# Optimization experiments

Hardware: AMD Instinct MI355X
Metric: run time of the kernel (lower is better)

The kernel has to match this reference:

```python
import jax, jax.numpy as jnp
import numpy as np

HEADS = 8


def setup_inputs() -> dict:
    key = jax.random.key(0)
    k1, k2, k3, k4, k5 = jax.random.split(key, 5)
    bt, b_sz, n, dim = 2, 4, 1024, 512
    inner6 = 3072  # inner_dim * 6 where inner_dim = heads * dim_head = 512
    return {
        "x": jax.random.normal(k1, (bt, b_sz, n, dim), dtype=jnp.float32),
        "W_qkv": jax.random.normal(k2, (dim, inner6), dtype=jnp.float32) * 0.02,
        "b_qkv": jax.random.normal(k3, (inner6,), dtype=jnp.float32) * 0.02,
        "W_out": jax.random.normal(k4, (1024, dim), dtype=jnp.float32) * 0.02,
        "b_out": jax.random.normal(k5, (dim,), dtype=jnp.float32) * 0.02,
    }


def reference(x, W_qkv, b_qkv, W_out, b_out):
    bt, b_sz, n, dim = x.shape
    # to_qkv: Linear(dim, 3072) -> reshape (bt,b,n,3,H,hd) -> transpose(2,4)
    qkv = (x @ W_qkv + b_qkv).reshape(bt, b_sz, n, 3, HEADS, -1)
    qkv = qkv.transpose(0, 1, 4, 3, 2, 5)  # (bt, b, H, 3, n, hd)
    q, k, v = qkv[:, :, :, 0], qkv[:, :, :, 1], qkv[:, :, :, 2]
    scale = (dim // HEADS) ** -0.5  # faithful: uses dim//heads, not per-head width
    attn = jax.nn.softmax(jnp.einsum("abhnd,abhmd->abhnm", q * scale, k), axis=-1)
    out = jnp.einsum("abhnm,abhmd->abhnd", attn, v)
    out = out.transpose(0, 1, 3, 2, 4).reshape(bt, b_sz, n, -1)  # (bt,b,n,H*hd)
    return out @ W_out + b_out
```

## Files before the change

kernel.cpp:

```cpp
#include <hip/hip_runtime.h>

typedef __attribute__((ext_vector_type(4))) float f32x4;
typedef __attribute__((ext_vector_type(16))) float f32x16;
typedef __attribute__((ext_vector_type(8))) __bf16 bf16x8;
typedef __attribute__((ext_vector_type(8))) unsigned short ushortx8;
typedef unsigned short u16;
typedef unsigned int u32;

#define AS1 __attribute__((address_space(1)))
#define AS3 __attribute__((address_space(3)))

__device__ __forceinline__ void gld_lds16(const void* g, void* s) {
  __builtin_amdgcn_global_load_lds((AS1 void*)g, (AS3 void*)s, 16, 0, 0);
}

__device__ __forceinline__ u16 f2bf(float f) {
  unsigned int u = __float_as_uint(f);
  unsigned int r = (u + 0x7FFFu + ((u >> 16) & 1u)) >> 16;
  return (u16)r;
}

#define QSCALE 0.1803368801111244f

__global__ void cvt_f32_bf16(const float* __restrict__ src, u16* __restrict__ dst, int n) {
  int i = (blockIdx.x * blockDim.x + threadIdx.x) * 8;
  if (i >= n) return;
  const float4 a = *(const float4*)&src[i];
  const float4 b = *(const float4*)&src[i + 4];
  ushortx8 o;
  o[0] = f2bf(a.x); o[1] = f2bf(a.y); o[2] = f2bf(a.z); o[3] = f2bf(a.w);
  o[4] = f2bf(b.x); o[5] = f2bf(b.y); o[6] = f2bf(b.z); o[7] = f2bf(b.w);
  *(ushortx8*)&dst[i] = o;
}

__global__ void scale_bias(const float* __restrict__ src, float* __restrict__ dst, int n,
                           int boundary, float s) {
  int i = blockIdx.x * blockDim.x + threadIdx.x;
  if (i < n) dst[i] = src[i] * (i < boundary ? s : 1.0f);
}

__global__ void transpose_to_bf16(const float* __restrict__ src, u16* __restrict__ dst,
                                  int R, int C, int boundary, float s) {
  __shared__ float tile[32][33];
  const int c0 = blockIdx.x * 32, r0 = blockIdx.y * 32;
  const int tx = threadIdx.x, ty = threadIdx.y;
  #pragma unroll
  for (int i = ty; i < 32; i += 8)
    tile[i][tx] = src[(size_t)(r0 + i) * C + c0 + tx];
  __syncthreads();
  #pragma unroll
  for (int i = ty; i < 32; i += 8) {
    const float sc = (c0 + i < boundary) ? s : 1.0f;
    dst[(size_t)(c0 + i) * R + r0 + tx] = f2bf(tile[tx][i] * sc);
  }
}

__global__ void transpose_v(const u16* __restrict__ qkv, u16* __restrict__ vt) {
  __shared__ u16 tile[32][34];
  const int bh = blockIdx.z, b = bh >> 3, h = bh & 7;
  const int n0 = blockIdx.y * 32, d0 = blockIdx.x * 32;
  const int tx = threadIdx.x, ty = threadIdx.y;
  const u16* src = qkv + (size_t)(b * 1024) * 3072 + 2048 + h * 128;
  #pragma unroll
  for (int i = ty; i < 32; i += 8)
    tile[i][tx] = src[(size_t)(n0 + i) * 3072 + d0 + tx];
  __syncthreads();
  u16* dst = vt + (size_t)(b * 8 + h) * 128 * 1024;
  #pragma unroll
  for (int i = ty; i < 32; i += 8)
    dst[(size_t)(d0 + i) * 1024 + n0 + tx] = tile[tx][i];
}

template <int BM, int BN, int BK, int OUT_BF16>
__global__ __launch_bounds__(256, 4) void gemm_bt(const u16* __restrict__ A,
                                                  const u16* __restrict__ Bt,
                                                  const float* __restrict__ bias,
                                                  void* __restrict__ Cv,
                                                  int M, int N, int K) {
  constexpr int RPC = 512 / BK;
  constexpr int LPR = BK / 8;
  constexpr int MASK = LPR - 1;
  constexpr int P = 64 / BK > 0 ? 64 / BK : 1;
  constexpr int CA = BM / RPC, CB = BN / RPC;
  constexpr int CAW = CA / 4, CBW = CB / 4;
  constexpr int VM = CAW + CBW;
  constexpr int FM = BM / 32, FN = BN / 32;
  constexpr int KS = BK / 32;

  __shared__ __attribute__((aligned(16))) u16 As[2][BM * BK];
  __shared__ __attribute__((aligned(16))) u16 Bs[2][BN * BK];
  const int nwg = gridDim.x * gridDim.y;
  int bid = blockIdx.y * gridDim.x + blockIdx.x;
  if ((nwg & 7) == 0) bid = (bid & 7) * (nwg >> 3) + (bid >> 3);
  const int n0 = (bid % gridDim.x) * BN, m0 = (bid / gridDim.x) * BM;
  const int tid = threadIdx.x;
  const int w = tid >> 6, l = tid & 63;
  const int wr = w >> 1, wc = w & 1;
  const int lr = l >> 4, lc = l & 15;
  f32x4 acc[FM][FN] = {};

#define GSTAGE(bi, k0)                                                          \
  do {                                                                          \
    _Pragma("unroll") for (int i = 0; i < CAW; ++i) {                           \
      const int c = w * CAW + i;                                                \
      const int row = c * RPC + l / LPR;                                        \
      const int col = ((l % LPR) ^ ((row / P) & MASK)) * 8;                     \
      gld_lds16(&A[(size_t)(m0 + row) * K + (k0) + col], &As[bi][c * 512]);     \
    }                                                                           \
    _Pragma("unroll") for (int i = 0; i < CBW; ++i) {                           \
      const int c = w * CBW + i;                                                \
      const int row = c * RPC + l / LPR;                                        \
      const int col = ((l % LPR) ^ ((row / P) & MASK)) * 8;                     \
      gld_lds16(&Bt[(size_t)(n0 + row) * K + (k0) + col], &Bs[bi][c * 512]);    \
    }                                                                           \
  } while (0)

#define GCOMP(bi)                                                                      \
  do {                                                                                 \
    _Pragma("unroll") for (int ks = 0; ks < KS; ++ks) {                                \
      bf16x8 af[FM], bfr[FN];                                                          \
      _Pragma("unroll") for (int m = 0; m < FM; ++m) {                                 \
        const int row = wr * (BM / 2) + m * 16 + lc;                                   \
        af[m] = *(const bf16x8*)&As[bi][row * BK +                                     \
                                        (((ks * 4 + lr) ^ ((row / P) & MASK)) << 3)];  \
      }                                                                                \
      _Pragma("unroll") for (int n = 0; n < FN; ++n) {                                 \
        const int row = wc * (BN / 2) + n * 16 + lc;                                   \
        bfr[n] = *(const bf16x8*)&Bs[bi][row * BK +                                    \
                                         (((ks * 4 + lr) ^ ((row / P) & MASK)) << 3)]; \
      }                                                                                \
      __builtin_amdgcn_s_setprio(1);                                                   \
      _Pragma("unroll") for (int m = 0; m < FM; ++m)                                   \
          _Pragma("unroll") for (int n = 0; n < FN; ++n)                               \
              acc[m][n] =                                                              \
          __builtin_amdgcn_mfma_f32_16x16x32_bf16(af[m], bfr[n], acc[m][n], 0, 0, 0);  \
      __builtin_amdgcn_s_setprio(0);                                                   \
    }                                                                                  \
  } while (0)

  GSTAGE(0, 0);
  int buf = 0;
  for (int k0 = BK; k0 < K; k0 += BK) {
    GSTAGE(buf ^ 1, k0);
    if constexpr (VM == 2)
      asm volatile("s_waitcnt vmcnt(2)" ::: "memory");
    else if constexpr (VM == 3)
      asm volatile("s_waitcnt vmcnt(3)" ::: "memory");
    else if constexpr (VM == 4)
      asm volatile("s_waitcnt vmcnt(4)" ::: "memory");
    else
      asm volatile("s_waitcnt vmcnt(8)" ::: "memory");
    __builtin_amdgcn_s_barrier();
    __builtin_amdgcn_sched_barrier(0);
    GCOMP(buf);
    __builtin_amdgcn_s_barrier();
    buf ^= 1;
  }
  asm volatile("s_waitcnt vmcnt(0)" ::: "memory");
  __builtin_amdgcn_s_barrier();
  __builtin_amdgcn_sched_barrier(0);
  GCOMP(buf);
#undef GSTAGE
#undef GCOMP

  #pragma unroll
  for (int n = 0; n < FN; ++n) {
    const int col = n0 + wc * (BN / 2) + n * 16 + lc;
    const float bv = bias[col];
    #pragma unroll
    for (int m = 0; m < FM; ++m) {
      #pragma unroll
      for (int r = 0; r < 4; ++r) {
        const int row = m0 + wr * (BM / 2) + m * 16 + lr * 4 + r;
        const float v = acc[m][n][r] + bv;
        if (OUT_BF16)
          ((u16*)Cv)[(size_t)row * N + col] = f2bf(v);
        else
          ((float*)Cv)[(size_t)row * N + col] = v;
      }
    }
  }
}

__global__ __launch_bounds__(512, 2) void gemm_qkv_8ph(const u16* __restrict__ A,
                                                       const u16* __restrict__ Bt,
                                                       const float* __restrict__ bias,
                                                       u16* __restrict__ C,
                                                       int M, int N, int K) {
  __shared__ __attribute__((aligned(16))) u16 SMEM[57344];
  u16* const AsP[2] = {SMEM, SMEM + 16384};
  u16* const BsP[2] = {SMEM + 32768, SMEM + 45056};
  const int nwg = gridDim.x;
  int bid = blockIdx.x;
  if ((nwg & 7) == 0) bid = (bid & 7) * (nwg >> 3) + (bid >> 3);
  const int ntile = N / 192;
  const int n0 = (bid % ntile) * 192, m0 = (bid / ntile) * 256;
  const int tid = threadIdx.x;
  const int w = tid >> 6, l = tid & 63;
  const int wr = w >> 2, wc = w & 3;
  const int lr = l >> 4, lc = l & 15;
  f32x4 acc[8][3] = {};
  bf16x8 af[2][2], bfv[3][2];

#define STAGE_A(bi, kt, h)                                                          \
  do {                                                                              \
    _Pragma("unroll") for (int cc = 0; cc < 2; ++cc) {                              \
      const int cib = (h) * 1024 + (cc * 8 + w) * 64;                               \
      const int ci = cib + l;                                                       \
      const int row = ci >> 3, ck = ci & 7;                                         \
      gld_lds16(&A[(size_t)(m0 + row) * K + (kt) * 64 + ((ck ^ (row & 7)) << 3)],   \
                &AsP[bi][cib * 8]);                                                 \
    }                                                                               \
  } while (0)

#define STAGE_B(bi, kt, t)                                                          \
  do {                                                                              \
    const int cib = (t) * 512 + w * 64;                                             \
    const int ci = cib + l;                                                         \
    const int row = ci >> 3, ck = ci & 7;                                           \
    gld_lds16(&Bt[(size_t)(n0 + row) * K + (kt) * 64 + ((ck ^ (row & 7)) << 3)],    \
              &BsP[bi][cib * 8]);                                                   \
  } while (0)

#define RD_A(bi, mp)                                                                \
  do {                                                                              \
    _Pragma("unroll") for (int m2 = 0; m2 < 2; ++m2)                                \
      _Pragma("unroll") for (int ks = 0; ks < 2; ++ks) {                            \
        const int row = wr * 128 + (2 * (mp) + m2) * 16 + lc;                       \
        af[m2][ks] = *(const bf16x8*)&AsP[bi][row * 64 +                            \
                                              (((ks * 4 + lr) ^ (lc & 7)) << 3)];   \
      }                                                                             \
  } while (0)

#define RD_B(bi)                                                                    \
  do {                                                                              \
    _Pragma("unroll") for (int n = 0; n < 3; ++n)                                   \
      _Pragma("unroll") for (int ks = 0; ks < 2; ++ks) {                            \
        const int row = wc * 48 + n * 16 + lc;                                      \
        bfv[n][ks] = *(const bf16x8*)&BsP[bi][row * 64 +                            \
                                              (((ks * 4 + lr) ^ (lc & 7)) << 3)];   \
      }                                                                             \
  } while (0)

#define MM(mp)                                                                      \
  do {                                                                              \
    __builtin_amdgcn_s_setprio(1);                                                  \
    _Pragma("unroll") for (int m2 = 0; m2 < 2; ++m2)                                \
      _Pragma("unroll") for (int n = 0; n < 3; ++n)                                 \
        _Pragma("unroll") for (int ks = 0; ks < 2; ++ks)                            \
          acc[2 * (mp) + m2][n] = __builtin_amdgcn_mfma_f32_16x16x32_bf16(          \
              af[m2][ks], bfv[n][ks], acc[2 * (mp) + m2][n], 0, 0, 0);              \
    __builtin_amdgcn_s_setprio(0);                                                  \
  } while (0)

#define BARC()                                                                      \
  do {                                                                              \
    __builtin_amdgcn_s_barrier();                                                   \
    asm volatile("s_waitcnt lgkmcnt(0)" ::: "memory");                              \
    __builtin_amdgcn_sched_barrier(0);                                              \
  } while (0)

  STAGE_B(0, 0, 0); STAGE_B(0, 0, 1); STAGE_B(0, 0, 2);
  STAGE_A(0, 0, 0); STAGE_A(0, 0, 1);
  STAGE_B(1, 1, 0); STAGE_B(1, 1, 1);
  asm volatile("s_waitcnt vmcnt(2)" ::: "memory");
  __builtin_amdgcn_s_barrier();
  __builtin_amdgcn_sched_barrier(0);

  const int NI = K >> 7;
  for (int i = 0; i < NI; ++i) {
    const bool nl = (i < NI - 1);
    const int tO = 2 * i + 1, tE2 = 2 * i + 2, tO2 = 2 * i + 3;
    RD_B(0); RD_A(0, 0);
    STAGE_B(1, tO, 2); STAGE_A(1, tO, 0); STAGE_A(1, tO, 1);
    BARC(); MM(0);
    __builtin_amdgcn_s_barrier();
    RD_A(0, 1);
    if (nl) STAGE_B(0, tE2, 0);
    BARC(); MM(1);
    __builtin_amdgcn_s_barrier();
    RD_A(0, 2);
    if (nl) STAGE_B(0, tE2, 1);
    BARC(); MM(2);
    __builtin_amdgcn_s_barrier();
    RD_A(0, 3);
    if (nl) STAGE_B(0, tE2, 2);
    BARC(); MM(3);
    if (nl) asm volatile("s_waitcnt vmcnt(3)" ::: "memory");
    else    asm volatile("s_waitcnt vmcnt(0)" ::: "memory");
    __builtin_amdgcn_s_barrier();
    __builtin_amdgcn_sched_barrier(0);
    RD_B(1); RD_A(1, 0);
    if (nl) STAGE_A(0, tE2, 0);
    BARC(); MM(0);
    __builtin_amdgcn_s_barrier();
    RD_A(1, 1);
    if (nl) STAGE_A(0, tE2, 1);
    BARC(); MM(1);
    __builtin_amdgcn_s_barrier();
    RD_A(1, 2);
    if (nl) STAGE_B(1, tO2, 0);
    BARC(); MM(2);
    __builtin_amdgcn_s_barrier();
    RD_A(1, 3);
    if (nl) STAGE_B(1, tO2, 1);
    BARC(); MM(3);
    if (nl) {
      asm volatile("s_waitcnt vmcnt(2)" ::: "memory");
      __builtin_amdgcn_s_barrier();
      __builtin_amdgcn_sched_barrier(0);
    }
  }
#undef STAGE_A
#undef STAGE_B
#undef RD_A
#undef RD_B
#undef MM
#undef BARC

  __builtin_amdgcn_s_barrier();
  #pragma unroll
  for (int n = 0; n < 3; ++n) {
    const float bv = bias[n0 + wc * 48 + n * 16 + lc];
    #pragma unroll
    for (int m = 0; m < 8; ++m) {
      #pragma unroll
      for (int r = 0; r < 4; ++r) {
        const int row = wr * 128 + m * 16 + lr * 4 + r;
        SMEM[row * 192 + wc * 48 + n * 16 + lc] = f2bf(acc[m][n][r] + bv);
      }
    }
  }
  __builtin_amdgcn_s_barrier();
  #pragma unroll
  for (int it = 0; it < 12; ++it) {
    const int chunk = it * 512 + tid;
    const int row = chunk / 24, c16 = chunk % 24;
    const bf16x8 v = *(const bf16x8*)&SMEM[row * 192 + c16 * 8];
    *(bf16x8*)&C[(size_t)(m0 + row) * N + n0 + c16 * 8] = v;
  }
}

__global__ __launch_bounds__(256, 2) void attn_fwd(const u16* __restrict__ qkv,
                                                   const u16* __restrict__ vt,
                                                   u16* __restrict__ attn_out) {
  __shared__ __attribute__((aligned(16))) u16 Ks[2][64 * 128];
  __shared__ __attribute__((aligned(16))) u16 Vs[2][64 * 128];
  const int orig = blockIdx.y * 8 + blockIdx.x;
  const int swz = (orig & 7) * 64 + (orig >> 3);
  const int bh = swz >> 3, b = bh >> 3, h = bh & 7;
  const int q0 = (swz & 7) * 128;
  const int tid = threadIdx.x, w = tid >> 6, l = tid & 63;
  const int ll = l & 31, hi = l >> 5;
  const int wq0 = q0 + w * 32;
  const u16* Qb = qkv + (size_t)(b * 1024 + wq0) * 3072 + h * 128;
  const u16* Kb = qkv + (size_t)(b * 1024) * 3072 + 1024 + h * 128;
  const u16* Vb = vt + (size_t)(b * 8 + h) * 128 * 1024;

  bf16x8 bq[8];
  #pragma unroll
  for (int s = 0; s < 8; ++s)
    bq[s] = *(const bf16x8*)&Qb[(size_t)ll * 3072 + s * 16 + hi * 8];
  asm volatile("s_waitcnt vmcnt(0)" ::: "memory");

  bf16x8 ones;
  #pragma unroll
  for (int i = 0; i < 8; ++i) ones[i] = (__bf16)1.0f;

  const u16* sb[8];
  int dst0;
  if (w < 2) {
    #pragma unroll
    for (int j = 0; j < 8; ++j) {
      const int r = w * 32 + j * 4 + (l >> 4);
      const int c = l & 15;
      sb[j] = Kb + (size_t)r * 3072 + ((c ^ (r & 15)) << 3);
    }
    dst0 = w * 4096;
  } else {
    #pragma unroll
    for (int j = 0; j < 8; ++j) {
      const int r2 = (w - 2) * 32 + j * 4 + (l >> 4);
      const int c = l & 15;
      const int d = ((c >> 3) ^ ((r2 >> 3) & 1)) * 64 + (r2 >> 5) * 32 + (r2 & 31);
      const int kc = (c & 7) ^ (r2 & 7);
      sb[j] = Vb + (size_t)d * 1024 + (kc << 3);
    }
    dst0 = (w - 2) * 4096;
  }

#define STAGE(bi, tt)                                                            \
  do {                                                                           \
    if (w < 2) {                                                                 \
      _Pragma("unroll") for (int j = 0; j < 8; ++j)                              \
          gld_lds16(sb[j] + (size_t)(tt)*196608, &Ks[bi][dst0 + j * 512]);       \
    } else {                                                                     \
      _Pragma("unroll") for (int j = 0; j < 8; ++j)                              \
          gld_lds16(sb[j] + (size_t)(tt)*64, &Vs[bi][dst0 + j * 512]);           \
    }                                                                            \
  } while (0)

#define QK(Kt)                                                                     \
  do {                                                                            \
    st0 = (f32x16){};                                                             \
    st1 = (f32x16){};                                                             \
    __builtin_amdgcn_s_setprio(1);                                                \
    _Pragma("unroll") for (int s = 0; s < 8; ++s) {                               \
      const int ch = ((s * 2 + hi) ^ (ll & 15)) << 3;                             \
      const bf16x8 ak0 = *(const bf16x8*)&(Kt)[ll * 128 + ch];                    \
      const bf16x8 ak1 = *(const bf16x8*)&(Kt)[(32 + ll) * 128 + ch];             \
      st0 = __builtin_amdgcn_mfma_f32_32x32x16_bf16(ak0, bq[s], st0, 0, 0, 0);    \
      st1 = __builtin_amdgcn_mfma_f32_32x32x16_bf16(ak1, bq[s], st1, 0, 0, 0);    \
    }                                                                             \
    __builtin_amdgcn_s_setprio(0);                                                \
  } while (0)

#define SOFTMAX()                                                                  \
  do {                                                                            \
    _Pragma("unroll") for (int kb = 0; kb < 2; ++kb) {                            \
      float pe[16];                                                               \
      _Pragma("unroll") for (int r = 0; r < 16; ++r)                              \
          pe[r] = exp2f(kb ? st1[r] : st0[r]);                                    \
      _Pragma("unroll") for (int j = 0; j < 8; ++j) {                             \
        u32 d_;                                                                   \
        asm("v_cvt_pk_bf16_f32 %0, %1, %2"                                        \
            : "=v"(d_)                                                            \
            : "v"(pe[2 * j]), "v"(pe[2 * j + 1]));                                \
        mm[kb * 8 + j] = d_;                                                      \
      }                                                                           \
      asm volatile("v_permlane32_swap_b32 %0, %1"                                 \
                   : "+v"(mm[kb * 8 + 0]), "+v"(mm[kb * 8 + 2]));                 \
      asm volatile("v_permlane32_swap_b32 %0, %1"                                 \
                   : "+v"(mm[kb * 8 + 1]), "+v"(mm[kb * 8 + 3]));                 \
      asm volatile("v_permlane32_swap_b32 %0, %1"                                 \
                   : "+v"(mm[kb * 8 + 4]), "+v"(mm[kb * 8 + 6]));                 \
      asm volatile("v_permlane32_swap_b32 %0, %1"                                 \
                   : "+v"(mm[kb * 8 + 5]), "+v"(mm[kb * 8 + 7]));                 \
    }                                                                             \
  } while (0)

#define PV(Vt_)                                                                    \
  do {                                                                            \
    __builtin_amdgcn_s_setprio(1);                                                \
    _Pragma("unroll") for (int kb = 0; kb < 2; ++kb) {                            \
      _Pragma("unroll") for (int s2 = 0; s2 < 2; ++s2) {                          \
        union { u32 u[4]; bf16x8 v; } pu;                                         \
        pu.u[0] = mm[kb * 8 + s2 * 4 + 0];                                        \
        pu.u[1] = mm[kb * 8 + s2 * 4 + 1];                                        \
        pu.u[2] = mm[kb * 8 + s2 * 4 + 2];                                        \
        pu.u[3] = mm[kb * 8 + s2 * 4 + 3];                                        \
        const bf16x8 pa = pu.v;                                                   \
        acc_l = __builtin_amdgcn_mfma_f32_32x32x16_bf16(pa, ones, acc_l, 0, 0, 0);\
        _Pragma("unroll") for (int db = 0; db < 4; ++db) {                        \
          const int r2 = (db & 1) * 32 + ll;                                      \
          const int c = ((((db >> 1) ^ ((ll >> 3) & 1)) << 3) |                   \
                         ((kb * 4 + s2 * 2 + hi) ^ (ll & 7)));                    \
          const bf16x8 bv = *(const bf16x8*)&(Vt_)[r2 * 128 + c * 8];             \
          acc_o[db] =                                                             \
              __builtin_amdgcn_mfma_f32_32x32x16_bf16(pa, bv, acc_o[db], 0, 0, 0);\
        }                                                                         \
      }                                                                           \
    }                                                                             \
    __builtin_amdgcn_s_setprio(0);                                                \
  } while (0)

  f32x16 acc_o[4] = {};
  f32x16 acc_l = {};
  f32x16 st0, st1;
  u32 mm[16];

  STAGE(0, 0);
  int buf = 0;
  for (int t = 0; t < 15; ++t) {
    STAGE(buf ^ 1, t + 1);
    asm volatile("s_waitcnt vmcnt(8)" ::: "memory");
    __builtin_amdgcn_s_barrier();
    __builtin_amdgcn_sched_barrier(0);
    QK(Ks[buf]);
    SOFTMAX();
    PV(Vs[buf]);
    __builtin_amdgcn_s_barrier();
    buf ^= 1;
  }
  asm volatile("s_waitcnt vmcnt(0)" ::: "memory");
  __builtin_amdgcn_s_barrier();
  __builtin_amdgcn_sched_barrier(0);
  QK(Ks[buf]);
  SOFTMAX();
  PV(Vs[buf]);

#undef STAGE
#undef QK
#undef SOFTMAX
#undef PV

  float inv[16];
  #pragma unroll
  for (int r = 0; r < 16; ++r) inv[r] = __builtin_amdgcn_rcpf(acc_l[r]);
  u16* Ob = attn_out + (size_t)(b * 1024 + wq0) * 1024 + h * 128;
  #pragma unroll
  for (int db = 0; db < 4; ++db)
    #pragma unroll
    for (int r = 0; r < 16; ++r) {
      const int q = (r & 3) + 8 * (r >> 2) + 4 * hi;
      Ob[(size_t)q * 1024 + db * 32 + ll] = f2bf(acc_o[db][r] * inv[r]);
    }
}

extern "C" void kernel_launch(void* const* d_in, const int* in_sizes, int n_in,
                              void* d_out, int out_size, void* d_ws, size_t ws_size,
                              hipStream_t stream) {
  const float* x = (const float*)d_in[0];
  const float* Wqkv = (const float*)d_in[1];
  const float* bqkv = (const float*)d_in[2];
  const float* Wout = (const float*)d_in[3];
  const float* bout = (const float*)d_in[4];
  float* out = (float*)d_out;

  char* ws = (char*)d_ws;
  u16* xb    = (u16*)(ws);
  u16* wqkvt = (u16*)(ws + 8388608);
  u16* woutt = (u16*)(ws + 8388608 + 3145728);
  u16* qkvb  = (u16*)(ws + 12582912);
  u16* vtb   = (u16*)(ws + 62914560);
  u16* aob   = (u16*)(ws + 79691776);
  float* bq2 = (float*)aob;

  cvt_f32_bf16<<<2048, 256, 0, stream>>>(x, xb, 8192 * 512);
  scale_bias<<<12, 256, 0, stream>>>(bqkv, bq2, 3072, 1024, QSCALE);
  transpose_to_bf16<<<dim3(96, 16), dim3(32, 8), 0, stream>>>(Wqkv, wqkvt, 512, 3072, 1024, QSCALE);
  transpose_to_bf16<<<dim3(16, 32), dim3(32, 8), 0, stream>>>(Wout, woutt, 1024, 512, 0, 1.0f);

  gemm_qkv_8ph<<<dim3(512), 512, 0, stream>>>(xb, wqkvt, bq2, qkvb, 8192, 3072, 512);

  transpose_v<<<dim3(4, 32, 64), dim3(32, 8), 0, stream>>>(qkvb, vtb);

  attn_fwd<<<dim3(8, 64), 256, 0, stream>>>(qkvb, vtb, aob);

  gemm_bt<128, 64, 32, 0><<<dim3(8, 64), 256, 0, stream>>>(aob, woutt, bout, out,
                                                           8192, 512, 1024);
}
```

Baseline: 132.6 us.

## Fuse prep kernels and write transposed V directly from QKV GEMM epilogue

The four preprocessing kernels (x conversion, bias scaling, two weight transposes) are merged into one launch that dispatches on block index. The separate V transpose kernel is removed: the QKV GEMM epilogue writes V columns straight into the transposed vt layout with 4-element vector stores, and skips storing V into the qkv buffer. This removes launch overhead and a full read and write of V, but the direct vt stores are narrower and strided compared with the staged 16-byte stores used for Q and K.

```diff
diff --git a/kernel.cpp b/kernel.cpp
--- a/kernel.cpp
+++ b/kernel.cpp
@@ -4,6 +4,7 @@
 typedef __attribute__((ext_vector_type(16))) float f32x16;
 typedef __attribute__((ext_vector_type(8))) __bf16 bf16x8;
 typedef __attribute__((ext_vector_type(8))) unsigned short ushortx8;
+typedef __attribute__((ext_vector_type(4))) unsigned short ushortx4;
 typedef unsigned short u16;
 typedef unsigned int u32;
 
@@ -22,53 +23,52 @@
 
 #define QSCALE 0.1803368801111244f
 
-__global__ void cvt_f32_bf16(const float* __restrict__ src, u16* __restrict__ dst, int n) {
-  int i = (blockIdx.x * blockDim.x + threadIdx.x) * 8;
-  if (i >= n) return;
-  const float4 a = *(const float4*)&src[i];
-  const float4 b = *(const float4*)&src[i + 4];
-  ushortx8 o;
-  o[0] = f2bf(a.x); o[1] = f2bf(a.y); o[2] = f2bf(a.z); o[3] = f2bf(a.w);
-  o[4] = f2bf(b.x); o[5] = f2bf(b.y); o[6] = f2bf(b.z); o[7] = f2bf(b.w);
-  *(ushortx8*)&dst[i] = o;
-}
-
-__global__ void scale_bias(const float* __restrict__ src, float* __restrict__ dst, int n,
-                           int boundary, float s) {
-  int i = blockIdx.x * blockDim.x + threadIdx.x;
-  if (i < n) dst[i] = src[i] * (i < boundary ? s : 1.0f);
-}
-
-__global__ void transpose_to_bf16(const float* __restrict__ src, u16* __restrict__ dst,
-                                  int R, int C, int boundary, float s) {
+__global__ __launch_bounds__(256) void prep_fused(
+    const float* __restrict__ x, u16* __restrict__ xb,
+    const float* __restrict__ bqkv, float* __restrict__ bq2,
+    const float* __restrict__ Wqkv, u16* __restrict__ wqkvt,
+    const float* __restrict__ Wout, u16* __restrict__ woutt) {
+  const int gid = blockIdx.x, tid = threadIdx.x;
+  if (gid < 2048) {
+    const int i = (gid * 256 + tid) * 8;
+    const float4 a = *(const float4*)&x[i];
+    const float4 b = *(const float4*)&x[i + 4];
+    ushortx8 o;
+    o[0] = f2bf(a.x); o[1] = f2bf(a.y); o[2] = f2bf(a.z); o[3] = f2bf(a.w);
+    o[4] = f2bf(b.x); o[5] = f2bf(b.y); o[6] = f2bf(b.z); o[7] = f2bf(b.w);
+    *(ushortx8*)&xb[i] = o;
+    return;
+  }
   __shared__ float tile[32][33];
-  const int c0 = blockIdx.x * 32, r0 = blockIdx.y * 32;
-  const int tx = threadIdx.x, ty = threadIdx.y;
-  #pragma unroll
-  for (int i = ty; i < 32; i += 8)
-    tile[i][tx] = src[(size_t)(r0 + i) * C + c0 + tx];
-  __syncthreads();
-  #pragma unroll
-  for (int i = ty; i < 32; i += 8) {
-    const float sc = (c0 + i < boundary) ? s : 1.0f;
-    dst[(size_t)(c0 + i) * R + r0 + tx] = f2bf(tile[tx][i] * sc);
-  }
-}
-
-__global__ void transpose_v(const u16* __restrict__ qkv, u16* __restrict__ vt) {
-  __shared__ u16 tile[32][34];
-  const int bh = blockIdx.z, b = bh >> 3, h = bh & 7;
-  const int n0 = blockIdx.y * 32, d0 = blockIdx.x * 32;
-  const int tx = threadIdx.x, ty = threadIdx.y;
-  const u16* src = qkv + (size_t)(b * 1024) * 3072 + 2048 + h * 128;
-  #pragma unroll
-  for (int i = ty; i < 32; i += 8)
-    tile[i][tx] = src[(size_t)(n0 + i) * 3072 + d0 + tx];
-  __syncthreads();
-  u16* dst = vt + (size_t)(b * 8 + h) * 128 * 1024;
-  #pragma unroll
-  for (int i = ty; i < 32; i += 8)
-    dst[(size_t)(d0 + i) * 1024 + n0 + tx] = tile[tx][i];
+  const int tx = tid & 31, ty = tid >> 5;
+  if (gid < 3584) {
+    const int t = gid - 2048;
+    const int c0 = (t % 96) * 32, r0 = (t / 96) * 32;
+    #pragma unroll
+    for (int i = ty; i < 32; i += 8)
+      tile[i][tx] = Wqkv[(size_t)(r0 + i) * 3072 + c0 + tx];
+    __syncthreads();
+    #pragma unroll
+    for (int i = ty; i < 32; i += 8) {
+      const float sc = (c0 + i < 1024) ? QSCALE : 1.0f;
+      wqkvt[(size_t)(c0 + i) * 512 + r0 + tx] = f2bf(tile[tx][i] * sc);
+    }
+    return;
+  }
+  if (gid < 4096) {
+    const int t = gid - 3584;
+    const int c0 = (t % 16) * 32, r0 = (t / 16) * 32;
+    #pragma unroll
+    for (int i = ty; i < 32; i += 8)
+      tile[i][tx] = Wout[(size_t)(r0 + i) * 512 + c0 + tx];
+    __syncthreads();
+    #pragma unroll
+    for (int i = ty; i < 32; i += 8)
+      woutt[(size_t)(c0 + i) * 1024 + r0 + tx] = f2bf(tile[tx][i]);
+    return;
+  }
+  const int i = (gid - 4096) * 256 + tid;
+  if (i < 3072) bq2[i] = bqkv[i] * (i < 1024 ? QSCALE : 1.0f);
 }
 
 template <int BM, int BN, int BK, int OUT_BF16>
@@ -186,6 +186,7 @@
                                                        const u16* __restrict__ Bt,
                                                        const float* __restrict__ bias,
                                                        u16* __restrict__ C,
+                                                       u16* __restrict__ vt,
                                                        int M, int N, int K) {
   __shared__ __attribute__((aligned(16))) u16 SMEM[57344];
   u16* const AsP[2] = {SMEM, SMEM + 16384};
@@ -319,15 +320,32 @@
 #undef BARC
 
   __builtin_amdgcn_s_barrier();
+  const int b_idx = m0 >> 10;
+  const int tok0 = m0 & 1023;
   #pragma unroll
   for (int n = 0; n < 3; ++n) {
-    const float bv = bias[n0 + wc * 48 + n * 16 + lc];
-    #pragma unroll
-    for (int m = 0; m < 8; ++m) {
+    const int gc = n0 + wc * 48 + n * 16 + lc;
+    const float bv = bias[gc];
+    if (gc < 2048) {
       #pragma unroll
-      for (int r = 0; r < 4; ++r) {
-        const int row = wr * 128 + m * 16 + lr * 4 + r;
-        SMEM[row * 192 + wc * 48 + n * 16 + lc] = f2bf(acc[m][n][r] + bv);
+      for (int m = 0; m < 8; ++m)
+        #pragma unroll
+        for (int r = 0; r < 4; ++r) {
+          const int row = wr * 128 + m * 16 + lr * 4 + r;
+          SMEM[row * 192 + wc * 48 + n * 16 + lc] = f2bf(acc[m][n][r] + bv);
+        }
+    } else {
+      const int hd = gc - 2048;
+      u16* vrow = vt + ((size_t)(b_idx * 8 + (hd >> 7)) * 128 + (hd & 127)) * 1024;
+      #pragma unroll
+      for (int m = 0; m < 8; ++m) {
+        const int tok = tok0 + wr * 128 + m * 16 + lr * 4;
+        ushortx4 o;
+        o[0] = f2bf(acc[m][n][0] + bv);
+        o[1] = f2bf(acc[m][n][1] + bv);
+        o[2] = f2bf(acc[m][n][2] + bv);
+        o[3] = f2bf(acc[m][n][3] + bv);
+        *(ushortx4*)&vrow[tok] = o;
       }
     }
   }
@@ -336,8 +354,10 @@
   for (int it = 0; it < 12; ++it) {
     const int chunk = it * 512 + tid;
     const int row = chunk / 24, c16 = chunk % 24;
-    const bf16x8 v = *(const bf16x8*)&SMEM[row * 192 + c16 * 8];
-    *(bf16x8*)&C[(size_t)(m0 + row) * N + n0 + c16 * 8] = v;
+    if (n0 + c16 * 8 < 2048) {
+      const bf16x8 v = *(const bf16x8*)&SMEM[row * 192 + c16 * 8];
+      *(bf16x8*)&C[(size_t)(m0 + row) * N + n0 + c16 * 8] = v;
+    }
   }
 }
 
@@ -526,14 +546,10 @@
   u16* aob   = (u16*)(ws + 79691776);
   float* bq2 = (float*)aob;
 
-  cvt_f32_bf16<<<2048, 256, 0, stream>>>(x, xb, 8192 * 512);
-  scale_bias<<<12, 256, 0, stream>>>(bqkv, bq2, 3072, 1024, QSCALE);
-  transpose_to_bf16<<<dim3(96, 16), dim3(32, 8), 0, stream>>>(Wqkv, wqkvt, 512, 3072, 1024, QSCALE);
-  transpose_to_bf16<<<dim3(16, 32), dim3(32, 8), 0, stream>>>(Wout, woutt, 1024, 512, 0, 1.0f);
-
-  gemm_qkv_8ph<<<dim3(512), 512, 0, stream>>>(xb, wqkvt, bq2, qkvb, 8192, 3072, 512);
-
-  transpose_v<<<dim3(4, 32, 64), dim3(32, 8), 0, stream>>>(qkvb, vtb);
+  prep_fused<<<4108, 256, 0, stream>>>(x, xb, bqkv, bq2, Wqkv, wqkvt, Wout, woutt);
+
+  gemm_qkv_8ph<<<dim3(512), 512, 0, stream>>>(xb, wqkvt, bq2, qkvb, vtb,
+                                              8192, 3072, 512);
 
   attn_fwd<<<dim3(8, 64), 256, 0, stream>>>(qkvb, vtb, aob);
 
```

Result: faster. 116.7 us (-11.9%).
